# Optimization experiments

Hardware: AMD Instinct MI355X
Metric: run time of the kernel (lower is better)

## Reference

```python
import jax, jax.numpy as jnp
import numpy as np

N_SCALES = 11
N_TAPS = 4
D4 = [0.4829629131445341, 0.8365163037378079, 0.2241438680420134, -0.1294095225512604]
B, N, D, H = 4, 2048, 1024, 16
HD = D // H  # 64


def setup_inputs() -> dict:
    key = jax.random.key(0)
    ks = jax.random.split(key, 8)
    s = 0.02
    return {
        "x": jax.random.normal(ks[0], (B, N, D), jnp.float32),
        "W_qkv": jax.random.normal(ks[1], (3 * D, D), jnp.float32) * s,
        "b_qkv": jnp.zeros((3 * D,), jnp.float32),
        "W_out": jax.random.normal(ks[2], (D, D), jnp.float32) * s,
        "b_out": jnp.zeros((D,), jnp.float32),
        "W_gate": jax.random.normal(ks[3], (D, D), jnp.float32) * s,
        "b_gate": jnp.full((D,), 2.0, jnp.float32),  # nn.init.constant_(gate bias, 2.0)
        "scale_gain": jax.random.normal(ks[4], (N_SCALES, H), jnp.float32) * 0.1,
        "W_qscale": jax.random.normal(ks[5], (N_SCALES, HD), jnp.float32) * 0.01,
        "identity_bypass": jnp.full((H,), -4.0, jnp.float32),
        "pos_bias": jax.random.normal(ks[6], (N_SCALES * N_TAPS, H), jnp.float32) * 0.01,
    }


def reference(x, W_qkv, b_qkv, W_out, b_out, W_gate, b_gate, scale_gain, W_qscale, identity_bypass, pos_bias):
    # qkv projection and head split -> [B,H,N,HD]
    qkv = x @ W_qkv.T + b_qkv
    q, k, v = jnp.split(qkv, 3, axis=-1)
    to_heads = lambda t: t.reshape(B, N, H, HD).transpose(0, 2, 1, 3)
    q, k, v = to_heads(q), to_heads(k), to_heads(v)

    # Q-conditioned per-scale gains: [B,H,N,n_scales]
    q_offset = jnp.einsum('bhnd,sd->bhns', q, W_qscale)
    prior = scale_gain.T[None, :, None, :]  # [1,H,1,S]
    gains = jax.nn.softmax(q_offset + prior, axis=-1)

    out = jnp.zeros((B, H, N, HD), q.dtype)
    z = jnp.zeros((B, H, N, 1), q.dtype)
    tap_idx = 0
    for j in range(N_SCALES):  # fixed small structural loop (44 taps total)
        d = 1 << j
        g_j = gains[..., j][..., None]  # [B,H,N,1]
        for tau, h_coef in enumerate(D4):
            offset = d * tau
            bias_jt = pos_bias[tap_idx].reshape(1, H, 1, 1)
            tap_idx += 1
            if offset != 0 and offset >= N:
                continue
            if offset == 0:
                k_s, v_s = k, v
            else:
                pad = jnp.zeros((B, H, offset, HD), k.dtype)
                k_s = jnp.concatenate([pad, k[:, :, :N - offset, :]], axis=2)
                v_s = jnp.concatenate([pad, v[:, :, :N - offset, :]], axis=2)
            qk_feat = jax.nn.elu(jnp.sum(q * k_s, -1, keepdims=True) + bias_jt) + 1.0
            out = out + (g_j * h_coef) * qk_feat * v_s
            z = z + g_j * abs(h_coef) * qk_feat

    # identity bypass (offset-0 local term)
    bypass = jax.nn.softplus(identity_bypass).reshape(1, H, 1, 1)
    local_ft = jax.nn.elu(jnp.sum(q * k, -1, keepdims=True)) + 1.0
    out = out + bypass * local_ft * v
    z = z + bypass * local_ft
    out = out / (z + 1e-06)

    gathered = out.transpose(0, 2, 1, 3).reshape(B, N, D)
    gate = jax.nn.sigmoid(x @ W_gate.T + b_gate)
    return (gathered * gate) @ W_out.T + b_out  # dropout p: eval mode -> identity
```

## Files before the change

### kernel.cpp

```cpp
#include <hip/hip_runtime.h>
#include <hip/hip_bf16.h>

#define PB 4
#define PN 2048
#define PD 1024
#define PH 16
#define PHD 64
#define NSC 11

typedef __attribute__((ext_vector_type(8))) short short8;
typedef __attribute__((ext_vector_type(4))) float floatx4;

#define AS1 __attribute__((address_space(1)))
#define AS3 __attribute__((address_space(3)))

static __device__ __forceinline__ unsigned short bf16bits(float f) {
    __hip_bfloat16 h = __float2bfloat16(f);
    return __builtin_bit_cast(unsigned short, h);
}

__global__ void cast_f32_to_bf16_v4(const float4* __restrict__ in,
                                    ushort4* __restrict__ out, int n4) {
    int i = blockIdx.x * blockDim.x + threadIdx.x;
    if (i < n4) {
        float4 v = in[i];
        ushort4 o;
        o.x = bf16bits(v.x);
        o.y = bf16bits(v.y);
        o.z = bf16bits(v.z);
        o.w = bf16bits(v.w);
        out[i] = o;
    }
}

__global__ void cast_weights(const float4* __restrict__ wqkv,
                             const float4* __restrict__ wgate,
                             const float4* __restrict__ wout,
                             ushort4* __restrict__ wcomb,
                             ushort4* __restrict__ woutb) {
    int i = blockIdx.x * blockDim.x + threadIdx.x;
    const int QKV4 = 3 * PD * PD / 4;
    const int G4 = PD * PD / 4;
    float4 v;
    ushort4* dst;
    if (i < QKV4) {
        v = wqkv[i];
        dst = wcomb + i;
    } else if (i < QKV4 + G4) {
        v = wgate[i - QKV4];
        dst = wcomb + i;
    } else {
        v = wout[i - QKV4 - G4];
        dst = woutb + (i - QKV4 - G4);
    }
    ushort4 o;
    o.x = bf16bits(v.x);
    o.y = bf16bits(v.y);
    o.z = bf16bits(v.z);
    o.w = bf16bits(v.w);
    *dst = o;
}

__global__ void gate_mul(const float4* __restrict__ att,
                         const float4* __restrict__ gatep,
                         ushort4* __restrict__ gated, int n4) {
    int i = blockIdx.x * blockDim.x + threadIdx.x;
    if (i < n4) {
        float4 a = att[i];
        float4 gp = gatep[i];
        ushort4 o;
        o.x = bf16bits(a.x / (1.f + __expf(-gp.x)));
        o.y = bf16bits(a.y / (1.f + __expf(-gp.y)));
        o.z = bf16bits(a.z / (1.f + __expf(-gp.z)));
        o.w = bf16bits(a.w / (1.f + __expf(-gp.w)));
        gated[i] = o;
    }
}

#define GBM 128
#define GBN 128
#define GBK 64

__global__ __launch_bounds__(256) void gemm_bt128(
    const __hip_bfloat16* __restrict__ A,
    const __hip_bfloat16* __restrict__ Bm,
    const float* __restrict__ b1,
    const float* __restrict__ b2,
    int split,
    float* __restrict__ out1, int N1,
    float* __restrict__ out2, int N2,
    int K) {
    __shared__ alignas(16) __hip_bfloat16 sA[GBM * GBK];
    __shared__ alignas(16) __hip_bfloat16 sB[GBN * GBK];

    const int tid = threadIdx.x;
    const int lane = tid & 63;
    const int wave = tid >> 6;
    const int wy = wave >> 1;
    const int wx = wave & 1;

    const int lrow8 = lane >> 3;
    const int lchunk = lane & 7;
    const int gchunk = lchunk ^ lrow8;

    const int r16 = lane & 15;
    const int qd = lane >> 4;
    const int sw = r16 & 7;

    floatx4 acc[4][4];
#pragma unroll
    for (int i = 0; i < 4; i++)
#pragma unroll
        for (int j = 0; j < 4; j++) acc[i][j] = (floatx4){0.f, 0.f, 0.f, 0.f};

    const size_t arow0 = (size_t)blockIdx.y * GBM;
    const size_t brow0 = (size_t)blockIdx.x * GBN;

    for (int k0 = 0; k0 < K; k0 += GBK) {
        __syncthreads();
#pragma unroll
        for (int half = 0; half < 4; half++) {
            const int rbase = wave * 8 + half * 32;
            const __hip_bfloat16* gA =
                A + (arow0 + rbase + lrow8) * K + k0 + gchunk * 8;
            __builtin_amdgcn_global_load_lds(
                (const AS1 unsigned int*)(const void*)gA,
                (AS3 unsigned int*)(void*)(sA + rbase * GBK), 16, 0, 0);
            const __hip_bfloat16* gB =
                Bm + (brow0 + rbase + lrow8) * K + k0 + gchunk * 8;
            __builtin_amdgcn_global_load_lds(
                (const AS1 unsigned int*)(const void*)gB,
                (AS3 unsigned int*)(void*)(sB + rbase * GBK), 16, 0, 0);
        }
        __syncthreads();

#pragma unroll
        for (int kk = 0; kk < 2; kk++) {
            short8 af[4], bf[4];
            const int cs = (qd + 4 * kk);
#pragma unroll
            for (int i = 0; i < 4; i++)
                af[i] = *(const short8*)(sA + (wy * 64 + i * 16 + r16) * GBK +
                                         ((cs ^ sw) * 8));
#pragma unroll
            for (int j = 0; j < 4; j++)
                bf[j] = *(const short8*)(sB + (wx * 64 + j * 16 + r16) * GBK +
                                         ((cs ^ sw) * 8));
#pragma unroll
            for (int i = 0; i < 4; i++)
#pragma unroll
                for (int j = 0; j < 4; j++)
                    acc[i][j] = __builtin_amdgcn_mfma_f32_16x16x32_bf16(
                        af[i], bf[j], acc[i][j], 0, 0, 0);
        }
    }

#pragma unroll
    for (int i = 0; i < 4; i++) {
#pragma unroll
        for (int j = 0; j < 4; j++) {
            const int colb = (int)brow0 + wx * 64 + j * 16 + r16;
            const bool first = colb < split;
            const float bb = first ? b1[colb] : b2[colb - split];
            float* dst = first ? out1 : out2;
            const int nn = first ? N1 : N2;
            const int cc = first ? colb : colb - split;
#pragma unroll
            for (int e = 0; e < 4; e++) {
                const size_t row = arow0 + wy * 64 + i * 16 + qd * 4 + e;
                dst[row * (size_t)nn + cc] = acc[i][j][e] + bb;
            }
        }
    }
}


static constexpr int OFFS[21] = {1, 2, 3, 4, 6, 8, 12, 16, 24, 32, 48,
                                 64, 96, 128, 192, 256, 384, 512, 768, 1024, 1536};
static constexpr int U1J[21] = {0, 0, 0, 1, 1, 2, 2, 3, 3, 4, 4,
                                5, 5, 6, 6, 7, 7, 8, 8, 9, 9};
static constexpr int U1T[21] = {1, 2, 3, 2, 3, 2, 3, 2, 3, 2, 3,
                                2, 3, 2, 3, 2, 3, 2, 3, 2, 3};
static constexpr int U2J[21] = {-1, 1, -1, 2, -1, 3, -1, 4, -1, 5, -1,
                                6, -1, 7, -1, 8, -1, 9, -1, 10, -1};

static __device__ __forceinline__ float red8(float s) {
    int t;
    t = __builtin_amdgcn_update_dpp(0, __builtin_bit_cast(int, s), 0xB1, 0xF, 0xF, true);
    s += __builtin_bit_cast(float, t);
    t = __builtin_amdgcn_update_dpp(0, __builtin_bit_cast(int, s), 0x4E, 0xF, 0xF, true);
    s += __builtin_bit_cast(float, t);
    t = __builtin_amdgcn_update_dpp(0, __builtin_bit_cast(int, s), 0x141, 0xF, 0xF, true);
    s += __builtin_bit_cast(float, t);
    return s;
}

__global__ __launch_bounds__(256) void attn_kernel(
    const float* __restrict__ qkv,
    const float* __restrict__ scale_gain,
    const float* __restrict__ W_qscale,
    const float* __restrict__ identity_bypass,
    const float* __restrict__ pos_bias,
    float* __restrict__ att) {
    const int lane = threadIdx.x & 63;
    const int p = lane >> 3;
    const int l = lane & 7;

    const int wg = blockIdx.x;
    const int swg = (wg & 7) * 512 + (wg >> 3);

    const int flat = (swg * 4 + (threadIdx.x >> 6)) * 8;
    const int n = (flat & (PN - 1)) + p;
    const int h = (flat >> 11) & (PH - 1);
    const int b = flat >> 15;

    const size_t base_bn = (size_t)b * PN;
    const int col = h * PHD + l * 8;

    const float* qp = qkv + (base_bn + n) * (3 * PD) + col;
    const float4 qa = *(const float4*)qp;
    const float4 qb = *(const float4*)(qp + 4);
    const float4 k0a = *(const float4*)(qp + PD);
    const float4 k0b = *(const float4*)(qp + PD + 4);
    const float4 v0a = *(const float4*)(qp + 2 * PD);
    const float4 v0b = *(const float4*)(qp + 2 * PD + 4);

    auto dot8 = [](float4 a0, float4 a1, float4 b0, float4 b1) {
        float s = a0.x * b0.x;
        s = fmaf(a0.y, b0.y, s);
        s = fmaf(a0.z, b0.z, s);
        s = fmaf(a0.w, b0.w, s);
        s = fmaf(a1.x, b1.x, s);
        s = fmaf(a1.y, b1.y, s);
        s = fmaf(a1.z, b1.z, s);
        s = fmaf(a1.w, b1.w, s);
        return red8(s);
    };

    const float dot0 = dot8(qa, qb, k0a, k0b);

    float g[NSC];
    float mx = -1e30f;
#pragma unroll
    for (int s = 0; s < NSC; s++) {
        const float* wp = W_qscale + s * PHD + l * 8;
        const float4 w0 = *(const float4*)wp;
        const float4 w1 = *(const float4*)(wp + 4);
        g[s] = dot8(qa, qb, w0, w1) + scale_gain[s * PH + h];
        mx = fmaxf(mx, g[s]);
    }
    float ssum = 0.f;
#pragma unroll
    for (int s = 0; s < NSC; s++) {
        g[s] = __expf(g[s] - mx);
        ssum += g[s];
    }
    const float inv = 1.f / ssum;
#pragma unroll
    for (int s = 0; s < NSC; s++) g[s] *= inv;

    const float D4c[4] = {0.4829629131445341f, 0.8365163037378079f,
                          0.2241438680420134f, -0.1294095225512604f};

    float4 o0, o1;
    float z;

    {
        const float bp = log1pf(__expf(identity_bypass[h]));
        const float f0 = (dot0 > 0.f ? dot0 : __expf(dot0) - 1.f) + 1.f;
        float wsum = bp * f0;
#pragma unroll
        for (int j = 0; j < NSC; j++) {
            const float xx = dot0 + pos_bias[(j * 4) * PH + h];
            const float feat = (xx > 0.f ? xx : __expf(xx) - 1.f) + 1.f;
            wsum = fmaf(g[j], D4c[0] * feat, wsum);
        }
        z = wsum;
        o0.x = wsum * v0a.x;
        o0.y = wsum * v0a.y;
        o0.z = wsum * v0a.z;
        o0.w = wsum * v0a.w;
        o1.x = wsum * v0b.x;
        o1.y = wsum * v0b.y;
        o1.z = wsum * v0b.z;
        o1.w = wsum * v0b.w;
    }

#pragma unroll
    for (int t = 0; t < 21; t++) {
        const int off = OFFS[t];
        const bool valid = (n >= off);
        const int idx = valid ? (n - off) : 0;
        const float vm = valid ? 1.f : 0.f;
        const size_t rb = (base_bn + idx) * (3 * PD);
        const float* kp = qkv + rb + PD + col;
        const float* vp = qkv + rb + 2 * PD + col;
        const float4 k4a = *(const float4*)kp;
        const float4 k4b = *(const float4*)(kp + 4);
        const float4 v4a = *(const float4*)vp;
        const float4 v4b = *(const float4*)(vp + 4);
        const float dv = dot8(qa, qb, k4a, k4b) * vm;

        float wv, zacc;
        {
            const int j = U1J[t], tau = U1T[t];
            const float xx = dv + pos_bias[(j * 4 + tau) * PH + h];
            const float feat = (xx > 0.f ? xx : __expf(xx) - 1.f) + 1.f;
            const float wp = g[j] * (D4c[tau] * feat);
            zacc = fabsf(wp);
            wv = wp;
        }
        if (U2J[t] >= 0) {
            const int j = U2J[t];
            const float xx = dv + pos_bias[(j * 4 + 1) * PH + h];
            const float feat = (xx > 0.f ? xx : __expf(xx) - 1.f) + 1.f;
            const float wp = g[j] * (D4c[1] * feat);
            zacc += wp;
            wv += wp;
        }
        z += zacc;
        wv *= vm;
        o0.x = fmaf(wv, v4a.x, o0.x);
        o0.y = fmaf(wv, v4a.y, o0.y);
        o0.z = fmaf(wv, v4a.z, o0.z);
        o0.w = fmaf(wv, v4a.w, o0.w);
        o1.x = fmaf(wv, v4b.x, o1.x);
        o1.y = fmaf(wv, v4b.y, o1.y);
        o1.z = fmaf(wv, v4b.z, o1.z);
        o1.w = fmaf(wv, v4b.w, o1.w);
    }

    const float zi = 1.f / (z + 1e-6f);
    float4 r0, r1;
    r0.x = o0.x * zi; r0.y = o0.y * zi; r0.z = o0.z * zi; r0.w = o0.w * zi;
    r1.x = o1.x * zi; r1.y = o1.y * zi; r1.z = o1.z * zi; r1.w = o1.w * zi;
    float* op = att + (base_bn + n) * PD + col;
    *(float4*)op = r0;
    *(float4*)(op + 4) = r1;
}

extern "C" void kernel_launch(void* const* d_in, const int* in_sizes, int n_in,
                              void* d_out, int out_size, void* d_ws, size_t ws_size,
                              hipStream_t stream) {
    const float* x = (const float*)d_in[0];
    const float* W_qkv = (const float*)d_in[1];
    const float* b_qkv = (const float*)d_in[2];
    const float* W_out = (const float*)d_in[3];
    const float* b_out = (const float*)d_in[4];
    const float* W_gate = (const float*)d_in[5];
    const float* b_gate = (const float*)d_in[6];
    const float* scale_gain = (const float*)d_in[7];
    const float* W_qscale = (const float*)d_in[8];
    const float* identity_bypass = (const float*)d_in[9];
    const float* pos_bias = (const float*)d_in[10];
    float* out = (float*)d_out;

    const int M = PB * PN;
    char* ws = (char*)d_ws;
    size_t off = 0;
    auto alloc = [&](size_t bytes) -> void* {
        void* p = ws + off;
        off += (bytes + 255) & ~(size_t)255;
        return p;
    };
    __hip_bfloat16* x_bf = (__hip_bfloat16*)alloc((size_t)M * PD * 2);
    __hip_bfloat16* wcomb_bf = (__hip_bfloat16*)alloc((size_t)4 * PD * PD * 2);
    __hip_bfloat16* wout_bf = (__hip_bfloat16*)alloc((size_t)PD * PD * 2);
    float* qkv = (float*)alloc((size_t)M * 3 * PD * 4);
    float* gate = (float*)alloc((size_t)M * PD * 4);
    float* att = (float*)alloc((size_t)M * PD * 4);
    __hip_bfloat16* gated = (__hip_bfloat16*)alloc((size_t)M * PD * 2);

    cast_f32_to_bf16_v4<<<(M * PD / 4) / 256, 256, 0, stream>>>(
        (const float4*)x, (ushort4*)x_bf, M * PD / 4);
    cast_weights<<<(5 * PD * PD / 4) / 256, 256, 0, stream>>>(
        (const float4*)W_qkv, (const float4*)W_gate, (const float4*)W_out,
        (ushort4*)wcomb_bf, (ushort4*)wout_bf);

    gemm_bt128<<<dim3(4 * PD / GBN, M / GBM), 256, 0, stream>>>(
        x_bf, wcomb_bf, b_qkv, b_gate, 3 * PD, qkv, 3 * PD, gate, PD, PD);

    attn_kernel<<<(PB * PH * PN) / 32, 256, 0, stream>>>(
        qkv, scale_gain, W_qscale, identity_bypass, pos_bias, att);

    gate_mul<<<(M * PD / 4) / 256, 256, 0, stream>>>(
        (const float4*)att, (const float4*)gate, (ushort4*)gated, M * PD / 4);

    gemm_bt128<<<dim3(PD / GBN, M / GBM), 256, 0, stream>>>(
        gated, wout_bf, b_out, b_out, PD, out, PD, out, PD, PD);
}
```

Measured before the change: 328.4 us.

## Add 256x256-tile 8-wave GEMM with double-buffered direct-to-LDS loads for QKV+gate

Adds a new bf16 GEMM kernel with 256x256 output tiles, 512 threads (8 waves, each computing 128x64), double-buffered LDS staging via global_load_lds, XOR-swizzled LDS layout, and MFMA issue interleaved with the prefetch of the next K tile under raised wave priority. It replaces the 128-tile GEMM only for the fused QKV+gate projection. The aim is to raise arithmetic intensity and hide global-load latency behind compute. In exchange it uses 128 KB of LDS and many accumulator registers per block, and launches only 16x32=512 blocks, which limits occupancy.

```diff
diff --git a/kernel.cpp b/kernel.cpp
--- a/kernel.cpp
+++ b/kernel.cpp
@@ -174,6 +174,181 @@
     }
 }
 
+#define TBM 256
+#define TBN 256
+#define TBK 64
+
+__global__ __launch_bounds__(512) void gemm_bt256(
+    const __hip_bfloat16* __restrict__ A,
+    const __hip_bfloat16* __restrict__ Bm,
+    const float* __restrict__ b1,
+    const float* __restrict__ b2,
+    int split,
+    float* __restrict__ out1, int N1,
+    float* __restrict__ out2, int N2,
+    int K) {
+    __shared__ alignas(16) __hip_bfloat16 sA[2 * TBM * TBK];
+    __shared__ alignas(16) __hip_bfloat16 sB[2 * TBN * TBK];
+
+    const int tid = threadIdx.x;
+    const int lane = tid & 63;
+    const int wid = tid >> 6;
+    const int wrow = wid >> 2;
+    const int wcol = wid & 3;
+
+    const int lrow8 = lane >> 3;
+    const int lchunk = lane & 7;
+    const int gchunk = lchunk ^ lrow8;
+
+    const int r16 = lane & 15;
+    const int qd = lane >> 4;
+    const int sw = r16 & 7;
+
+    const size_t arow0 = (size_t)blockIdx.y * TBM;
+    const size_t brow0 = (size_t)blockIdx.x * TBN;
+
+    const int nt = K >> 6;
+    const size_t rowskip = (size_t)64 * K;
+
+    const __hip_bfloat16* gA = A + (arow0 + wid * 8 + lrow8) * (size_t)K + gchunk * 8;
+    const __hip_bfloat16* gB = Bm + (brow0 + wid * 8 + lrow8) * (size_t)K + gchunk * 8;
+    const int ldsAb = wid * 8 * TBK;
+
+    auto stage = [&](int cc, int ktn) {
+#pragma unroll
+        for (int rd = 0; rd < 4; ++rd) {
+            __builtin_amdgcn_global_load_lds(
+                (const AS1 unsigned int*)(const void*)(gA + (size_t)rd * rowskip + ktn * TBK),
+                (AS3 unsigned int*)(void*)(sA + cc * (TBM * TBK) + ldsAb + rd * (64 * TBK)),
+                16, 0, 0);
+            __builtin_amdgcn_global_load_lds(
+                (const AS1 unsigned int*)(const void*)(gB + (size_t)rd * rowskip + ktn * TBK),
+                (AS3 unsigned int*)(void*)(sB + cc * (TBN * TBK) + ldsAb + rd * (64 * TBK)),
+                16, 0, 0);
+        }
+    };
+
+    floatx4 acc[8][4];
+#pragma unroll
+    for (int i = 0; i < 8; i++)
+#pragma unroll
+        for (int j = 0; j < 4; j++) acc[i][j] = (floatx4){0.f, 0.f, 0.f, 0.f};
+
+    const int aofs = (wrow * 128 + r16) * TBK;
+    const int bofs = (wcol * 64 + r16) * TBK;
+    const int ck0 = ((qd ^ sw) * 8);
+    const int ck1 = (((qd + 4) ^ sw) * 8);
+
+    stage(0, 0);
+    stage(1, 1);
+    asm volatile("s_waitcnt vmcnt(8)" ::: "memory");
+    __builtin_amdgcn_s_barrier();
+
+#pragma unroll 1
+    for (int kt = 0; kt < nt; ++kt) {
+        const int c = kt & 1;
+        const __hip_bfloat16* sAc = sA + c * (TBM * TBK);
+        const __hip_bfloat16* sBc = sB + c * (TBN * TBK);
+
+        short8 afr[8][2], bfr[4][2];
+
+#pragma unroll
+        for (int f = 0; f < 2; ++f) {
+            bfr[f][0] = *(const short8*)(sBc + bofs + f * 1024 + ck0);
+            bfr[f][1] = *(const short8*)(sBc + bofs + f * 1024 + ck1);
+        }
+#pragma unroll
+        for (int f = 0; f < 4; ++f) {
+            afr[f][0] = *(const short8*)(sAc + aofs + f * 1024 + ck0);
+            afr[f][1] = *(const short8*)(sAc + aofs + f * 1024 + ck1);
+        }
+        __builtin_amdgcn_s_setprio(1);
+#pragma unroll
+        for (int i = 0; i < 4; ++i)
+#pragma unroll
+            for (int j = 0; j < 2; ++j)
+#pragma unroll
+                for (int kk = 0; kk < 2; ++kk)
+                    acc[i][j] = __builtin_amdgcn_mfma_f32_16x16x32_bf16(
+                        afr[i][kk], bfr[j][kk], acc[i][j], 0, 0, 0);
+        __builtin_amdgcn_s_setprio(0);
+
+#pragma unroll
+        for (int f = 2; f < 4; ++f) {
+            bfr[f][0] = *(const short8*)(sBc + bofs + f * 1024 + ck0);
+            bfr[f][1] = *(const short8*)(sBc + bofs + f * 1024 + ck1);
+        }
+#pragma unroll
+        for (int f = 4; f < 8; ++f) {
+            afr[f][0] = *(const short8*)(sAc + aofs + f * 1024 + ck0);
+            afr[f][1] = *(const short8*)(sAc + aofs + f * 1024 + ck1);
+        }
+        __builtin_amdgcn_s_setprio(1);
+#pragma unroll
+        for (int i = 0; i < 4; ++i)
+#pragma unroll
+            for (int j = 2; j < 4; ++j)
+#pragma unroll
+            for (int kk = 0; kk < 2; ++kk)
+                    acc[i][j] = __builtin_amdgcn_mfma_f32_16x16x32_bf16(
+                        afr[i][kk], bfr[j][kk], acc[i][j], 0, 0, 0);
+        __builtin_amdgcn_s_setprio(0);
+
+        asm volatile("s_waitcnt lgkmcnt(0)" ::: "memory");
+        __builtin_amdgcn_sched_barrier(0);
+        __builtin_amdgcn_s_barrier();
+
+        if (kt + 2 < nt) stage(c, kt + 2);
+
+        __builtin_amdgcn_s_setprio(1);
+#pragma unroll
+        for (int i = 4; i < 8; ++i)
+#pragma unroll
+            for (int j = 0; j < 2; ++j)
+#pragma unroll
+                for (int kk = 0; kk < 2; ++kk)
+                    acc[i][j] = __builtin_amdgcn_mfma_f32_16x16x32_bf16(
+                        afr[i][kk], bfr[j][kk], acc[i][j], 0, 0, 0);
+        __builtin_amdgcn_s_setprio(0);
+
+        __builtin_amdgcn_s_setprio(1);
+#pragma unroll
+        for (int i = 4; i < 8; ++i)
+#pragma unroll
+            for (int j = 2; j < 4; ++j)
+#pragma unroll
+                for (int kk = 0; kk < 2; ++kk)
+                    acc[i][j] = __builtin_amdgcn_mfma_f32_16x16x32_bf16(
+                        afr[i][kk], bfr[j][kk], acc[i][j], 0, 0, 0);
+        __builtin_amdgcn_s_setprio(0);
+
+        if (kt + 2 < nt) {
+            asm volatile("s_waitcnt vmcnt(8)" ::: "memory");
+        } else if (kt + 1 < nt) {
+            asm volatile("s_waitcnt vmcnt(0)" ::: "memory");
+        }
+        if (kt + 1 < nt) __builtin_amdgcn_s_barrier();
+    }
+
+#pragma unroll
+    for (int i = 0; i < 8; i++) {
+#pragma unroll
+        for (int j = 0; j < 4; j++) {
+            const int colb = (int)brow0 + wcol * 64 + j * 16 + r16;
+            const bool first = colb < split;
+            const float bb = first ? b1[colb] : b2[colb - split];
+            float* dst = first ? out1 : out2;
+            const int nn = first ? N1 : N2;
+            const int cc = first ? colb : colb - split;
+#pragma unroll
+            for (int e = 0; e < 4; e++) {
+                const size_t row = arow0 + wrow * 128 + i * 16 + qd * 4 + e;
+                dst[row * (size_t)nn + cc] = acc[i][j][e] + bb;
+            }
+        }
+    }
+}
+
 
 static constexpr int OFFS[21] = {1, 2, 3, 4, 6, 8, 12, 16, 24, 32, 48,
                                  64, 96, 128, 192, 256, 384, 512, 768, 1024, 1536};
@@ -377,7 +552,7 @@
         (const float4*)W_qkv, (const float4*)W_gate, (const float4*)W_out,
         (ushort4*)wcomb_bf, (ushort4*)wout_bf);
 
-    gemm_bt128<<<dim3(4 * PD / GBN, M / GBM), 256, 0, stream>>>(
+    gemm_bt256<<<dim3(4 * PD / TBN, M / TBM), 512, 0, stream>>>(
         x_bf, wcomb_bf, b_qkv, b_gate, 3 * PD, qkv, 3 * PD, gate, PD, PD);
 
     attn_kernel<<<(PB * PH * PN) / 32, 256, 0, stream>>>(
```

After: 303.9 us. 1.08x faster.
